# Kernel optimization log

Hardware: AMD Instinct MI355X
Metric: run time of the kernel (lower is better)

The kernel has to match this reference:

```python
import jax, jax.numpy as jnp
import numpy as np

LN_EPS = 1e-5


def setup_inputs() -> dict:
    key = jax.random.key(0)
    k1, k2, k3 = jax.random.split(key, 3)
    B, L, D = 4096, 200, 128
    padded_embeddings = jax.random.normal(k1, (B, L, D), dtype=jnp.float32)
    lengths = jnp.maximum(jax.random.randint(k2, (B,), 0, L), 1).astype(jnp.int64)
    w_att = jax.random.normal(k3, (D,), dtype=jnp.float32) * (1.0 / np.sqrt(D))
    b_att = jnp.zeros((1,), dtype=jnp.float32)
    ln_gamma = jnp.ones((D,), dtype=jnp.float32)
    ln_beta = jnp.zeros((D,), dtype=jnp.float32)
    return {
        "padded_embeddings": padded_embeddings,
        "lengths": lengths,
        "w_att": w_att,
        "b_att": b_att,
        "ln_gamma": ln_gamma,
        "ln_beta": ln_beta,
    }


def reference(padded_embeddings, lengths, w_att, b_att, ln_gamma, ln_beta):
    # attention scores: Linear(D, 1) then squeeze -> [B, L]
    scores = jnp.einsum("bld,d->bl", padded_embeddings, w_att) + b_att[0]
    L = padded_embeddings.shape[1]
    mask = jnp.arange(L)[None, :] < lengths[:, None]          # [B, L]
    scores = jnp.where(mask, scores, -jnp.inf)
    attn = jax.nn.softmax(scores, axis=-1)                    # [B, L]
    pooled = jnp.einsum("bld,bl->bd", padded_embeddings, attn)  # [B, D]
    # dropout is identity in eval mode; layernorm over last dim
    mu = jnp.mean(pooled, axis=-1, keepdims=True)
    var = jnp.var(pooled, axis=-1, keepdims=True)
    normed = (pooled - mu) * jax.lax.rsqrt(var + LN_EPS)
    return normed * ln_gamma + ln_beta
```

## Files before the change

### kernel.cpp

```cpp
#include <hip/hip_runtime.h>
#include <cfloat>
#include <cmath>

#define LN_EPS 1e-5f

constexpr int L = 200;
constexpr int D = 128;

__global__ __launch_bounds__(512, 4)
void fue_kernel(const float* __restrict__ emb,
                const int*   __restrict__ lengths,
                const float* __restrict__ w_att,
                const float* __restrict__ b_att,
                const float* __restrict__ gamma,
                const float* __restrict__ beta,
                float* __restrict__ out) {
    const int b    = blockIdx.x;
    const int tid  = threadIdx.x;
    const int wave = tid >> 6;
    const int lane = tid & 63;
    const int hw   = tid >> 5;
    const int hl   = tid & 31;

    __shared__ __align__(16) unsigned short row16[L * D];
    __shared__ float att[L];
    __shared__ float partial[16][D];
    __shared__ float red[16];

    const int   len  = lengths[b];
    const float bias = b_att[0];
    const float4 wv  = ((const float4*)w_att)[hl];
    const float* row = emb + (size_t)b * (L * D);

    const int iters = (len + 15) >> 4;

    for (int i = 0; i < iters; ++i) {
        const int l = hw + (i << 4);
        if (l < len) {
            const float4 x = *(const float4*)(row + l * D + hl * 4);

            unsigned bx = __float_as_uint(x.x), by = __float_as_uint(x.y);
            unsigned bz = __float_as_uint(x.z), bw = __float_as_uint(x.w);
            bx = (bx + 0x7fffu + ((bx >> 16) & 1u)) >> 16;
            by = (by + 0x7fffu + ((by >> 16) & 1u)) >> 16;
            bz = (bz + 0x7fffu + ((bz >> 16) & 1u)) >> 16;
            bw = (bw + 0x7fffu + ((bw >> 16) & 1u)) >> 16;
            uint2 pk = make_uint2(bx | (by << 16), bz | (bw << 16));
            *(uint2*)&row16[l * D + hl * 4] = pk;

            float s = x.x * wv.x + x.y * wv.y + x.z * wv.z + x.w * wv.w;
            s += __shfl_xor(s, 1);
            s += __shfl_xor(s, 2);
            s += __shfl_xor(s, 4);
            s += __shfl_xor(s, 8);
            s += __shfl_xor(s, 16);
            if (hl == 0) att[l] = s + bias;
        }
    }
    __syncthreads();

    float v = (tid < len) ? att[tid] : -FLT_MAX;
    float m = v;
    m = fmaxf(m, __shfl_xor(m, 1));
    m = fmaxf(m, __shfl_xor(m, 2));
    m = fmaxf(m, __shfl_xor(m, 4));
    m = fmaxf(m, __shfl_xor(m, 8));
    m = fmaxf(m, __shfl_xor(m, 16));
    m = fmaxf(m, __shfl_xor(m, 32));
    if (lane == 0) red[wave] = m;
    __syncthreads();
    m = red[0];
    #pragma unroll
    for (int k = 1; k < 8; ++k) m = fmaxf(m, red[k]);

    const float e = (tid < len) ? __expf(v - m) : 0.0f;
    if (tid < L) att[tid] = e;

    float s = e;
    s += __shfl_xor(s, 1);
    s += __shfl_xor(s, 2);
    s += __shfl_xor(s, 4);
    s += __shfl_xor(s, 8);
    s += __shfl_xor(s, 16);
    s += __shfl_xor(s, 32);
    if (lane == 0) red[8 + wave] = s;
    __syncthreads();
    float tot = red[8];
    #pragma unroll
    for (int k = 1; k < 8; ++k) tot += red[8 + k];
    const float inv = 1.0f / tot;

    float4 acc = make_float4(0.f, 0.f, 0.f, 0.f);
    for (int i = 0; i < iters; ++i) {
        const int l = hw + (i << 4);
        if (l < len) {
            const float a = att[l] * inv;
            const uint2 pk = *(const uint2*)&row16[l * D + hl * 4];
            const float x0 = __uint_as_float(pk.x << 16);
            const float x1 = __uint_as_float(pk.x & 0xffff0000u);
            const float x2 = __uint_as_float(pk.y << 16);
            const float x3 = __uint_as_float(pk.y & 0xffff0000u);
            acc.x += a * x0;
            acc.y += a * x1;
            acc.z += a * x2;
            acc.w += a * x3;
        }
    }
    *(float4*)&partial[hw][hl * 4] = acc;
    __syncthreads();

    float p = 0.f;
    if (tid < D) {
        #pragma unroll
        for (int g = 0; g < 16; ++g) p += partial[g][tid];
    }
    float s1 = p, s2 = p * p;
    s1 += __shfl_xor(s1, 1);  s2 += __shfl_xor(s2, 1);
    s1 += __shfl_xor(s1, 2);  s2 += __shfl_xor(s2, 2);
    s1 += __shfl_xor(s1, 4);  s2 += __shfl_xor(s2, 4);
    s1 += __shfl_xor(s1, 8);  s2 += __shfl_xor(s2, 8);
    s1 += __shfl_xor(s1, 16); s2 += __shfl_xor(s2, 16);
    s1 += __shfl_xor(s1, 32); s2 += __shfl_xor(s2, 32);
    if (lane == 0 && wave < 2) { red[wave] = s1; red[2 + wave] = s2; }
    __syncthreads();

    if (tid < D) {
        const float mu   = (red[0] + red[1]) * (1.0f / D);
        const float var  = (red[2] + red[3]) * (1.0f / D) - mu * mu;
        const float rstd = rsqrtf(var + LN_EPS);
        out[(size_t)b * D + tid] = (p - mu) * rstd * gamma[tid] + beta[tid];
    }
}

extern "C" void kernel_launch(void* const* d_in, const int* in_sizes, int n_in,
                              void* d_out, int out_size, void* d_ws, size_t ws_size,
                              hipStream_t stream) {
    const float* emb     = (const float*)d_in[0];
    const int*   lengths = (const int*)d_in[1];
    const float* w_att   = (const float*)d_in[2];
    const float* b_att   = (const float*)d_in[3];
    const float* gamma   = (const float*)d_in[4];
    const float* beta    = (const float*)d_in[5];
    float* out = (float*)d_out;

    const int B = in_sizes[1];
    fue_kernel<<<B, 512, 0, stream>>>(emb, lengths, w_att, b_att, gamma, beta, out);
}
```

Measured before the change: 514.0 us.

## Keep row embeddings in registers instead of bf16 shared memory staging

Removes the 51KB bf16 shared-memory buffer and instead holds up to 13 float4 rows per thread in registers across the score, softmax and pooling phases. Each row is loaded from global memory once, with all loads issued up front, and pooling now uses full fp32 values rather than bf16-rounded ones. This drops the LDS writes and reads and the bf16 conversion, and the lower LDS use may let more blocks fit per CU. The cost is about 52 extra VGPRs per thread, which under launch_bounds(512,4) may cause spills or limit occupancy.

```diff
diff --git a/kernel.cpp b/kernel.cpp
--- a/kernel.cpp
+++ b/kernel.cpp
@@ -4,8 +4,9 @@
 
 #define LN_EPS 1e-5f
 
-constexpr int L = 200;
-constexpr int D = 128;
+constexpr int L    = 200;
+constexpr int D    = 128;
+constexpr int JMAX = 13;
 
 __global__ __launch_bounds__(512, 4)
 void fue_kernel(const float* __restrict__ emb,
@@ -22,7 +23,6 @@
     const int hw   = tid >> 5;
     const int hl   = tid & 31;
 
-    __shared__ __align__(16) unsigned short row16[L * D];
     __shared__ float att[L];
     __shared__ float partial[16][D];
     __shared__ float red[16];
@@ -32,23 +32,19 @@
     const float4 wv  = ((const float4*)w_att)[hl];
     const float* row = emb + (size_t)b * (L * D);
 
-    const int iters = (len + 15) >> 4;
+    float4 x[JMAX];
+    #pragma unroll
+    for (int j = 0; j < JMAX; ++j) {
+        const int l = hw + (j << 4);
+        if (l < len)
+            x[j] = *(const float4*)(row + l * D + hl * 4);
+    }
 
-    for (int i = 0; i < iters; ++i) {
-        const int l = hw + (i << 4);
+    #pragma unroll
+    for (int j = 0; j < JMAX; ++j) {
+        const int l = hw + (j << 4);
         if (l < len) {
-            const float4 x = *(const float4*)(row + l * D + hl * 4);
-
-            unsigned bx = __float_as_uint(x.x), by = __float_as_uint(x.y);
-            unsigned bz = __float_as_uint(x.z), bw = __float_as_uint(x.w);
-            bx = (bx + 0x7fffu + ((bx >> 16) & 1u)) >> 16;
-            by = (by + 0x7fffu + ((by >> 16) & 1u)) >> 16;
-            bz = (bz + 0x7fffu + ((bz >> 16) & 1u)) >> 16;
-            bw = (bw + 0x7fffu + ((bw >> 16) & 1u)) >> 16;
-            uint2 pk = make_uint2(bx | (by << 16), bz | (bw << 16));
-            *(uint2*)&row16[l * D + hl * 4] = pk;
-
-            float s = x.x * wv.x + x.y * wv.y + x.z * wv.z + x.w * wv.w;
+            float s = x[j].x * wv.x + x[j].y * wv.y + x[j].z * wv.z + x[j].w * wv.w;
             s += __shfl_xor(s, 1);
             s += __shfl_xor(s, 2);
             s += __shfl_xor(s, 4);
@@ -91,19 +87,15 @@
     const float inv = 1.0f / tot;
 
     float4 acc = make_float4(0.f, 0.f, 0.f, 0.f);
-    for (int i = 0; i < iters; ++i) {
-        const int l = hw + (i << 4);
+    #pragma unroll
+    for (int j = 0; j < JMAX; ++j) {
+        const int l = hw + (j << 4);
         if (l < len) {
             const float a = att[l] * inv;
-            const uint2 pk = *(const uint2*)&row16[l * D + hl * 4];
-            const float x0 = __uint_as_float(pk.x << 16);
-            const float x1 = __uint_as_float(pk.x & 0xffff0000u);
-            const float x2 = __uint_as_float(pk.y << 16);
-            const float x3 = __uint_as_float(pk.y & 0xffff0000u);
-            acc.x += a * x0;
-            acc.y += a * x1;
-            acc.z += a * x2;
-            acc.w += a * x3;
+            acc.x += a * x[j].x;
+            acc.y += a * x[j].y;
+            acc.z += a * x[j].z;
+            acc.w += a * x[j].w;
         }
     }
     *(float4*)&partial[hw][hl * 4] = acc;
```

Result: no change. 506.7 us (-1.4%).
